# Performance work log

Measured on AMD Instinct MI355X. Metric: run time of the kernel, lower is better.

The kernel has to match this reference:

```python
import jax, jax.numpy as jnp
import numpy as np

N = 50000      # total nodes
E = 800000     # directed edges
G = 512        # graphs in batch
F_IN = 64      # node feature dim
H = 128        # hidden dim
L = 3          # gnn layers
OUT = 12       # tox21 tasks
EPS = 1e-5


def layer_norm(h, gamma, beta):
    mu = jnp.mean(h, axis=-1, keepdims=True)
    var = jnp.mean(jnp.square(h - mu), axis=-1, keepdims=True)
    return (h - mu) * jax.lax.rsqrt(var + EPS) * gamma + beta


def setup_inputs() -> dict:
    key = jax.random.key(0)
    ks = jax.random.split(key, 20)
    x = jax.random.normal(ks[0], (N, F_IN), jnp.float32)
    edge_index = jax.random.randint(ks[1], (2, E), 0, N, dtype=jnp.int64)
    batch_ids = jnp.sort(jax.random.randint(ks[2], (N,), 0, G, dtype=jnp.int64))
    s_in = 1.0 / np.sqrt(F_IN)
    s_h = 1.0 / np.sqrt(H)
    return {
        "x": x,
        "edge_index": edge_index,
        "batch_ids": batch_ids,
        "W_embed": jax.random.normal(ks[3], (F_IN, H), jnp.float32) * s_in,
        "b_embed": jnp.zeros((H,), jnp.float32),
        "g_embed": jnp.ones((H,), jnp.float32),
        "be_embed": jnp.zeros((H,), jnp.float32),
        "W_conv": jax.random.normal(ks[4], (L, H, H), jnp.float32) * s_h,
        "b_conv": jnp.zeros((L, H), jnp.float32),
        "g_ln": jnp.ones((L, H), jnp.float32),
        "b_ln": jnp.zeros((L, H), jnp.float32),
        "W_r1": jax.random.normal(ks[5], (H, H // 2), jnp.float32) * s_h,
        "b_r1": jnp.zeros((H // 2,), jnp.float32),
        "W_r2": jax.random.normal(ks[6], (H // 2, OUT), jnp.float32) * (1.0 / np.sqrt(H // 2)),
        "b_r2": jnp.zeros((OUT,), jnp.float32),
    }


def reference(x, edge_index, batch_ids, W_embed, b_embed, g_embed, be_embed,
              W_conv, b_conv, g_ln, b_ln, W_r1, b_r1, W_r2, b_r2):
    n = x.shape[0]
    # node embedding: Linear -> LayerNorm -> ReLU (dropout = eval identity)
    h = jax.nn.relu(layer_norm(x @ W_embed + b_embed, g_embed, be_embed))

    # GCN normalization with self-loops (PyG GCNConv semantics)
    loop = jnp.arange(n, dtype=edge_index.dtype)
    src = jnp.concatenate([edge_index[0], loop])  # message sources
    dst = jnp.concatenate([edge_index[1], loop])  # message targets
    deg = jax.ops.segment_sum(jnp.ones_like(dst, dtype=h.dtype), dst, num_segments=N)
    dinv = jnp.where(deg > 0, jax.lax.rsqrt(deg), 0.0)
    norm = dinv[src] * dinv[dst]  # [E+N]

    for i in range(L):
        h_prev = h
        m = h @ W_conv[i]                                        # [N,H] linear first
        msg = m[src] * norm[:, None]                             # gather + scale
        agg = jax.ops.segment_sum(msg, dst, num_segments=N)      # scatter-add
        agg = agg + b_conv[i]                                    # bias after aggregation
        h = jax.nn.relu(layer_norm(agg, g_ln[i], b_ln[i])) + h_prev  # norm+relu+residual

    # global mean pooling per graph
    counts = jax.ops.segment_sum(jnp.ones((n,), h.dtype), batch_ids, num_segments=G)
    pooled = jax.ops.segment_sum(h, batch_ids, num_segments=G) / jnp.maximum(counts, 1.0)[:, None]

    # readout MLP
    r = jax.nn.relu(pooled @ W_r1 + b_r1)
    return r @ W_r2 + b_r2
```

## Files before the change

### kernel.cpp

```cpp
#include <hip/hip_runtime.h>

#define HDIM 128
#define FIN 64
#define EPS 1e-5f
#define ECH 2048
#define PITCH 64

typedef unsigned int uint;
typedef unsigned short ushort;
typedef __attribute__((ext_vector_type(8))) short bf16x8;
typedef __attribute__((ext_vector_type(4))) float f32x4;

__device__ __forceinline__ ushort f2bf(float f) {
    uint u = __float_as_uint(f);
    return (ushort)((u + 0x7fffu + ((u >> 16) & 1u)) >> 16);
}
__device__ __forceinline__ float bflo(uint u) { return __uint_as_float(u << 16); }
__device__ __forceinline__ float bfhi(uint u) { return __uint_as_float(u & 0xffff0000u); }

#define PART_OF(d) (((d) >> 4) & 7)

__global__ __launch_bounds__(256) void embed_fused(
    const float* __restrict__ x, const float* __restrict__ W,
    const float* __restrict__ b, const float* __restrict__ g,
    const float* __restrict__ be, ushort* __restrict__ hbf, int nrows,
    const int* __restrict__ src, const int* __restrict__ dst,
    int* __restrict__ fcnt, ushort* __restrict__ ell, int e,
    const float* __restrict__ Wc, ushort* __restrict__ Wt)
{
    int t = threadIdx.x;
    int gtid = blockIdx.x * 256 + t;
    if (gtid < 3 * HDIM * HDIM) {
        int l = gtid >> 14, rem = gtid & 16383;
        int k = rem >> 7, nn = rem & 127;
        Wt[(l << 14) + nn * HDIM + k] = f2bf(Wc[gtid]);
    }
    {
        int gpart = blockIdx.x & 7;
        int base2 = ((blockIdx.x >> 3) * ECH) >> 1;
        const int2* dst2 = (const int2*)dst;
        const int2* src2 = (const int2*)src;
#pragma unroll
        for (int i = 0; i < ECH / 2 / 256; i++) {
            int idx2 = base2 + t + i * 256;
            if (idx2 * 2 < e) {
                int2 dd = dst2[idx2];
                int2 ss = src2[idx2];
                if (PART_OF(dd.x) == gpart) {
                    int slot = atomicAdd(&fcnt[dd.x], 1);
                    if (slot < PITCH) ell[((size_t)dd.x << 6) + slot] = (ushort)ss.x;
                }
                if (idx2 * 2 + 1 < e && PART_OF(dd.y) == gpart) {
                    int slot = atomicAdd(&fcnt[dd.y], 1);
                    if (slot < PITCH) ell[((size_t)dd.y << 6) + slot] = (ushort)ss.y;
                }
            }
        }
    }

    int row0 = blockIdx.x * 32;
    if (row0 >= nrows) return;

    __shared__ ushort Ws[FIN * HDIM];
    __shared__ ushort xs[32 * FIN];
    {
        const float4* W4 = (const float4*)W;
        ushort4* Ws4 = (ushort4*)Ws;
#pragma unroll
        for (int i = 0; i < (FIN * HDIM / 4) / 256; i++) {
            float4 v = W4[t + i * 256];
            ushort4 o = { f2bf(v.x), f2bf(v.y), f2bf(v.z), f2bf(v.w) };
            Ws4[t + i * 256] = o;
        }
    }
    int nr = nrows - row0; if (nr > 32) nr = 32;
    {
        const float4* x4 = (const float4*)(x + (size_t)row0 * FIN);
        ushort4* xs4 = (ushort4*)xs;
        for (int i = t; i < nr * (FIN / 4); i += 256) {
            float4 v = x4[i];
            ushort4 o = { f2bf(v.x), f2bf(v.y), f2bf(v.z), f2bf(v.w) };
            xs4[i] = o;
        }
    }
    __syncthreads();

    int c = (t & 31) * 4;
    int r0 = (t >> 5) * 4;
    float acc[4][4];
    float4 bv = *(const float4*)(b + c);
#pragma unroll
    for (int i = 0; i < 4; i++) { acc[i][0] = bv.x; acc[i][1] = bv.y; acc[i][2] = bv.z; acc[i][3] = bv.w; }
#pragma unroll 8
    for (int k = 0; k < FIN; k++) {
        uint2 wu = *(const uint2*)(Ws + k * HDIM + c);
        float w0 = bflo(wu.x), w1 = bfhi(wu.x), w2 = bflo(wu.y), w3 = bfhi(wu.y);
#pragma unroll
        for (int i = 0; i < 4; i++) {
            float xv = __uint_as_float((uint)xs[(r0 + i) * FIN + k] << 16);
            acc[i][0] += xv * w0; acc[i][1] += xv * w1;
            acc[i][2] += xv * w2; acc[i][3] += xv * w3;
        }
    }
    float4 gv = *(const float4*)(g + c);
    float4 bev = *(const float4*)(be + c);
#pragma unroll
    for (int i = 0; i < 4; i++) {
        float s1 = acc[i][0] + acc[i][1] + acc[i][2] + acc[i][3];
        float s2 = acc[i][0]*acc[i][0] + acc[i][1]*acc[i][1] + acc[i][2]*acc[i][2] + acc[i][3]*acc[i][3];
#pragma unroll
        for (int m = 16; m; m >>= 1) { s1 += __shfl_xor(s1, m); s2 += __shfl_xor(s2, m); }
        float mu = s1 * (1.0f / HDIM);
        float var = s2 * (1.0f / HDIM) - mu * mu;
        float rstd = rsqrtf(var + EPS);
        int row = row0 + r0 + i;
        if (row < nrows) {
            float ox = fmaxf((acc[i][0] - mu) * rstd * gv.x + bev.x, 0.f);
            float oy = fmaxf((acc[i][1] - mu) * rstd * gv.y + bev.y, 0.f);
            float oz = fmaxf((acc[i][2] - mu) * rstd * gv.z + bev.z, 0.f);
            float ow = fmaxf((acc[i][3] - mu) * rstd * gv.w + bev.w, 0.f);
            uint2 hb;
            hb.x = ((uint)f2bf(oy) << 16) | f2bf(ox);
            hb.y = ((uint)f2bf(ow) << 16) | f2bf(oz);
            *(uint2*)(hbf + (size_t)row * HDIM + c) = hb;
        }
    }
}

__global__ __launch_bounds__(256) void gemm_mfma_kernel(
    const ushort* __restrict__ hbf, const ushort* __restrict__ Wt,
    const int* __restrict__ fcnt, ushort* __restrict__ mbf, int nrows)
{
    __shared__ ushort ws[64 * HDIM];
    int t = threadIdx.x;
    int wid = t >> 6, lane = t & 63;
    int row0 = (blockIdx.x >> 1) * 64;
    int colh = (blockIdx.x & 1) * 64;

#pragma unroll
    for (int it = 0; it < 4; it++) {
        int chunk = t * 4 + it;
        int r = chunk >> 4;
        int offb = (chunk & 15) * 16;
        uint4 d = *(const uint4*)(Wt + (size_t)(colh + r) * HDIM + (offb >> 1));
        *(uint4*)((char*)ws + r * 256 + (offb ^ ((r & 7) << 4))) = d;
    }

    int arow = row0 + wid * 16 + (lane & 15);
    int arcl = (arow < nrows) ? arow : (nrows - 1);
    int kgrp = lane >> 4;
    const ushort* aptr = hbf + (size_t)arcl * HDIM + kgrp * 8;
    bf16x8 af[4];
#pragma unroll
    for (int ks = 0; ks < 4; ks++)
        af[ks] = *(const bf16x8*)(aptr + ks * 32);

    __syncthreads();

    f32x4 acc[4];
#pragma unroll
    for (int nt = 0; nt < 4; nt++) acc[nt] = (f32x4){0.f, 0.f, 0.f, 0.f};

    int kgb = kgrp * 16;
#pragma unroll
    for (int ks = 0; ks < 4; ks++) {
        int kb = ks * 64 + kgb;
#pragma unroll
        for (int nt = 0; nt < 4; nt++) {
            int nrow = nt * 16 + (lane & 15);
            bf16x8 bfrag = *(const bf16x8*)((const char*)ws + nrow * 256 + (kb ^ ((nrow & 7) << 4)));
            acc[nt] = __builtin_amdgcn_mfma_f32_16x16x32_bf16(af[ks], bfrag, acc[nt], 0, 0, 0);
        }
    }

    int rbase = row0 + wid * 16 + ((lane >> 4) << 2);
#pragma unroll
    for (int q = 0; q < 4; q++) {
        int grow = rbase + q;
        if (grow < nrows) {
            float dv = rsqrtf((float)(fcnt[grow] + 1));
            ushort* orow = mbf + (size_t)grow * HDIM + colh + (lane & 15);
#pragma unroll
            for (int nt = 0; nt < 4; nt++)
                orow[nt * 16] = f2bf(acc[nt][q] * dv);
        }
    }
}

__global__ __launch_bounds__(256) void agg_kernel(
    const ushort* __restrict__ mbf, const ushort* __restrict__ ell, const int* __restrict__ fcnt,
    const float* __restrict__ bc,
    const float* __restrict__ gl, const float* __restrict__ bl,
    const ushort* __restrict__ hbf_in, ushort* __restrict__ hbf_out, int n)
{
    int wave = threadIdx.x >> 6, lane = threadIdx.x & 63;
    int v = blockIdx.x * 4 + wave;
    if (v >= n) return;
    const uint* m1 = (const uint*)mbf;
    uint hp = ((const uint*)hbf_in)[(size_t)v * 64 + lane];
    uint aa = m1[(size_t)v * 64 + lane];
    float ax = bflo(aa), ay = bfhi(aa);
    int deg = fcnt[v];
    const ushort* row = ell + ((size_t)v << 6);
    for (int base = 0; base < deg; base += 64) {
        int idx = base + lane;
        int my = (idx < deg) ? (int)row[idx] : 0;
        int cc = deg - base; if (cc > 64) cc = 64;
        int i = 0;
        for (; i + 4 <= cc; i += 4) {
            int u0 = __shfl(my, i);
            int u1 = __shfl(my, i + 1);
            int u2 = __shfl(my, i + 2);
            int u3 = __shfl(my, i + 3);
            uint w0 = m1[(size_t)u0 * 64 + lane];
            uint w1 = m1[(size_t)u1 * 64 + lane];
            uint w2 = m1[(size_t)u2 * 64 + lane];
            uint w3 = m1[(size_t)u3 * 64 + lane];
            ax += bflo(w0); ay += bfhi(w0);
            ax += bflo(w1); ay += bfhi(w1);
            ax += bflo(w2); ay += bfhi(w2);
            ax += bflo(w3); ay += bfhi(w3);
        }
        for (; i < cc; ++i) {
            int u0 = __shfl(my, i);
            uint w0 = m1[(size_t)u0 * 64 + lane];
            ax += bflo(w0); ay += bfhi(w0);
        }
    }
    float dvv = rsqrtf((float)(deg + 1));
    float2 bcv = ((const float2*)bc)[lane];
    float vx = ax * dvv + bcv.x;
    float vy = ay * dvv + bcv.y;
    float s1v = vx + vy, s2v = vx * vx + vy * vy;
#pragma unroll
    for (int m = 32; m; m >>= 1) { s1v += __shfl_xor(s1v, m); s2v += __shfl_xor(s2v, m); }
    float mu = s1v * (1.f / 128.f);
    float var = s2v * (1.f / 128.f) - mu * mu;
    float rstd = rsqrtf(var + EPS);
    float2 gv = ((const float2*)gl)[lane];
    float2 blv = ((const float2*)bl)[lane];
    float ox = fmaxf((vx - mu) * rstd * gv.x + blv.x, 0.f) + bflo(hp);
    float oy = fmaxf((vy - mu) * rstd * gv.y + blv.y, 0.f) + bfhi(hp);
    ((uint*)hbf_out)[(size_t)v * 64 + lane] = ((uint)f2bf(oy) << 16) | f2bf(ox);
}

__global__ __launch_bounds__(256) void pool_readout(
    const ushort* __restrict__ hbf, const int* __restrict__ batch,
    const float* __restrict__ W1, const float* __restrict__ b1,
    const float* __restrict__ W2, const float* __restrict__ b2,
    float* __restrict__ out, int n, int G)
{
    int g = blockIdx.x, t = threadIdx.x;
    int lo = 0, hi = n;
    while (lo < hi) { int mid = (lo + hi) >> 1; if (batch[mid] < g) lo = mid + 1; else hi = mid; }
    int lo2 = lo, hi2 = n;
    while (lo2 < hi2) { int mid = (lo2 + hi2) >> 1; if (batch[mid] < g + 1) lo2 = mid + 1; else hi2 = mid; }
    int cp = t & 63, portion = t >> 6;
    float accx = 0.f, accy = 0.f;
    const uint* h1 = (const uint*)hbf;
    for (int nd = lo + portion; nd < lo2; nd += 4) {
        uint u = h1[(size_t)nd * 64 + cp];
        accx += bflo(u); accy += bfhi(u);
    }
    float cntf = (float)(lo2 - lo); if (cntf < 1.f) cntf = 1.f;
    __shared__ float psx[256], psy[256];
    __shared__ float ps[HDIM];
    __shared__ float rs[64];
    psx[t] = accx; psy[t] = accy;
    __syncthreads();
    if (t < 64) {
        float px = psx[t] + psx[t + 64] + psx[t + 128] + psx[t + 192];
        float py = psy[t] + psy[t + 64] + psy[t + 128] + psy[t + 192];
        ps[2 * t]     = px / cntf;
        ps[2 * t + 1] = py / cntf;
    }
    __syncthreads();
    if (t < 64) {
        float a = b1[t];
#pragma unroll 4
        for (int k = 0; k < HDIM; k++) a += ps[k] * W1[k * 64 + t];
        rs[t] = fmaxf(a, 0.f);
    }
    __syncthreads();
    if (t < 12) {
        float a = b2[t];
#pragma unroll
        for (int k = 0; k < 64; k++) a += rs[k] * W2[k * 12 + t];
        out[(size_t)g * 12 + t] = a;
    }
}

extern "C" void kernel_launch(void* const* d_in, const int* in_sizes, int n_in,
                              void* d_out, int out_size, void* d_ws, size_t ws_size,
                              hipStream_t stream) {
    const float* x       = (const float*)d_in[0];
    const int*   ei      = (const int*)d_in[1];
    const int*   batch   = (const int*)d_in[2];
    const float* W_embed = (const float*)d_in[3];
    const float* b_embed = (const float*)d_in[4];
    const float* g_embed = (const float*)d_in[5];
    const float* be_emb  = (const float*)d_in[6];
    const float* W_conv  = (const float*)d_in[7];
    const float* b_conv  = (const float*)d_in[8];
    const float* g_ln    = (const float*)d_in[9];
    const float* b_ln    = (const float*)d_in[10];
    const float* W_r1    = (const float*)d_in[11];
    const float* b_r1    = (const float*)d_in[12];
    const float* W_r2    = (const float*)d_in[13];
    const float* b_r2    = (const float*)d_in[14];
    float* out = (float*)d_out;

    int N = in_sizes[2];
    int E = in_sizes[1] / 2;
    int G = out_size / 12;
    int npad = ((N + 255) / 256) * 256;

    char* w = (char*)d_ws;
    ushort* hbf0 = (ushort*)w;  w += (size_t)N * HDIM * 2;
    ushort* hbf1 = (ushort*)w;  w += (size_t)N * HDIM * 2;
    ushort* mbf  = (ushort*)w;  w += (size_t)N * HDIM * 2;
    ushort* Wt   = (ushort*)w;  w += (size_t)3 * HDIM * HDIM * 2;
    int* fcnt    = (int*)w;     w += (size_t)npad * 4;
    ushort* ell  = (ushort*)w;  w += (size_t)npad * PITCH * 2;

    int nchunks = (E + ECH - 1) / ECH;
    int gridEC = nchunks * 8;
    int gemmBlocks = ((N + 63) / 64) * 2;

    hipMemsetAsync(fcnt, 0, (size_t)npad * 4, stream);

    embed_fused<<<gridEC, 256, 0, stream>>>(
        x, W_embed, b_embed, g_embed, be_emb, hbf0, N,
        ei, ei + E, fcnt, ell, E, W_conv, Wt);

    const ushort* hin = hbf0;
    ushort* hout = hbf1;
    for (int l = 0; l < 3; l++) {
        gemm_mfma_kernel<<<gemmBlocks, 256, 0, stream>>>(
            hin, Wt + (size_t)l * HDIM * HDIM, fcnt, mbf, N);
        agg_kernel<<<(N + 3) / 4, 256, 0, stream>>>(
            mbf, ell, fcnt, b_conv + l * HDIM, g_ln + l * HDIM, b_ln + l * HDIM,
            hin, hout, N);
        ushort* tmp = (ushort*)hin; hin = hout; hout = tmp;
    }
    pool_readout<<<G, 256, 0, stream>>>(hbf1 == hout ? hbf0 : hbf1, batch, W_r1, b_r1, W_r2, b_r2, out, N, G);
}
```

Before: 219.5 us.

## Build ELL adjacency via two-pass LDS counting sort instead of global atomics

Replaces the per-edge global atomicAdd on fcnt with a two-pass scheme. Pass one counts destinations per (chunk, partition) in shared memory. A scan kernel computes per-chunk base offsets and degrees, and pass two fills the ELL slots using LDS atomics, fused with the first-layer GEMM. This removes the memset and contended global atomics, and makes slot order deterministic. The cost is an extra kernel launch, extra count/base buffers, and two reads of the dst array.

Measured after the change: 256.0 us. 16.6% more time.

```diff
diff --git a/kernel.cpp b/kernel.cpp
--- a/kernel.cpp
+++ b/kernel.cpp
@@ -3,8 +3,9 @@
 #define HDIM 128
 #define FIN 64
 #define EPS 1e-5f
-#define ECH 2048
 #define PITCH 64
+#define NSUB 32
+#define NFB 256
 
 typedef unsigned int uint;
 typedef unsigned short ushort;
@@ -19,50 +20,45 @@
 __device__ __forceinline__ float bfhi(uint u) { return __uint_as_float(u & 0xffff0000u); }
 
 #define PART_OF(d) (((d) >> 4) & 7)
-
-__global__ __launch_bounds__(256) void embed_fused(
+#define DLOCAL(d)  (((((d) >> 7)) << 4) | ((d) & 15))
+
+__global__ __launch_bounds__(256) void embed_pass1(
     const float* __restrict__ x, const float* __restrict__ W,
     const float* __restrict__ b, const float* __restrict__ g,
     const float* __restrict__ be, ushort* __restrict__ hbf, int nrows,
-    const int* __restrict__ src, const int* __restrict__ dst,
-    int* __restrict__ fcnt, ushort* __restrict__ ell, int e,
+    const int* __restrict__ dst, int* __restrict__ cnt32, int e, int chunkLen, int DL,
     const float* __restrict__ Wc, ushort* __restrict__ Wt)
 {
+    extern __shared__ char smem[];
     int t = threadIdx.x;
-    int gtid = blockIdx.x * 256 + t;
-    if (gtid < 3 * HDIM * HDIM) {
-        int l = gtid >> 14, rem = gtid & 16383;
-        int k = rem >> 7, nn = rem & 127;
-        Wt[(l << 14) + nn * HDIM + k] = f2bf(Wc[gtid]);
-    }
-    {
-        int gpart = blockIdx.x & 7;
-        int base2 = ((blockIdx.x >> 3) * ECH) >> 1;
-        const int2* dst2 = (const int2*)dst;
-        const int2* src2 = (const int2*)src;
-#pragma unroll
-        for (int i = 0; i < ECH / 2 / 256; i++) {
-            int idx2 = base2 + t + i * 256;
-            if (idx2 * 2 < e) {
-                int2 dd = dst2[idx2];
-                int2 ss = src2[idx2];
-                if (PART_OF(dd.x) == gpart) {
-                    int slot = atomicAdd(&fcnt[dd.x], 1);
-                    if (slot < PITCH) ell[((size_t)dd.x << 6) + slot] = (ushort)ss.x;
-                }
-                if (idx2 * 2 + 1 < e && PART_OF(dd.y) == gpart) {
-                    int slot = atomicAdd(&fcnt[dd.y], 1);
-                    if (slot < PITCH) ell[((size_t)dd.y << 6) + slot] = (ushort)ss.y;
-                }
-            }
-        }
-    }
-
-    int row0 = blockIdx.x * 32;
+
+    if ((int)blockIdx.x < NFB) {
+        int gtid = blockIdx.x * 256 + t;
+        if (gtid < 3 * HDIM * HDIM) {
+            int l = gtid >> 14, rem = gtid & 16383;
+            int k = rem >> 7, nn = rem & 127;
+            Wt[(l << 14) + nn * HDIM + k] = f2bf(Wc[gtid]);
+        }
+        int* cnt = (int*)smem;
+        for (int i = t; i < DL; i += 256) cnt[i] = 0;
+        __syncthreads();
+        int gp = blockIdx.x & 7, s = blockIdx.x >> 3;
+        int beg = s * chunkLen, end = beg + chunkLen; if (end > e) end = e;
+        for (int idx = beg + t; idx < end; idx += 256) {
+            int d = dst[idx];
+            if (PART_OF(d) == gp) atomicAdd(&cnt[DLOCAL(d)], 1);
+        }
+        __syncthreads();
+        int* outp = cnt32 + (size_t)blockIdx.x * DL;
+        for (int i = t; i < DL; i += 256) outp[i] = cnt[i];
+        return;
+    }
+
+    int row0 = ((int)blockIdx.x - NFB) * 32;
     if (row0 >= nrows) return;
 
-    __shared__ ushort Ws[FIN * HDIM];
-    __shared__ ushort xs[32 * FIN];
+    ushort* Ws = (ushort*)smem;
+    ushort* xs = (ushort*)(smem + 16384);
     {
         const float4* W4 = (const float4*)W;
         ushort4* Ws4 = (ushort4*)Ws;
@@ -127,15 +123,33 @@
     }
 }
 
-__global__ __launch_bounds__(256) void gemm_mfma_kernel(
+__global__ __launch_bounds__(256) void scan_b(
+    const int* __restrict__ cnt32, int* __restrict__ base32,
+    int* __restrict__ fcnt, int n, int DL)
+{
+    int d = blockIdx.x * 256 + threadIdx.x;
+    if (d >= n) return;
+    int gp = PART_OF(d), dl = DLOCAL(d);
+    int run = 0;
+#pragma unroll
+    for (int s = 0; s < NSUB; s++) {
+        size_t off = (size_t)((s << 3) | gp) * DL + dl;
+        int cv = cnt32[off];
+        base32[off] = run;
+        run += cv;
+    }
+    fcnt[d] = run;
+}
+
+__device__ __forceinline__ void gemm_body(
     const ushort* __restrict__ hbf, const ushort* __restrict__ Wt,
-    const int* __restrict__ fcnt, ushort* __restrict__ mbf, int nrows)
-{
-    __shared__ ushort ws[64 * HDIM];
+    const int* __restrict__ fcnt, ushort* __restrict__ mbf, int nrows,
+    int bid, ushort* ws)
+{
     int t = threadIdx.x;
     int wid = t >> 6, lane = t & 63;
-    int row0 = (blockIdx.x >> 1) * 64;
-    int colh = (blockIdx.x & 1) * 64;
+    int row0 = (bid >> 1) * 64;
+    int colh = (bid & 1) * 64;
 
 #pragma unroll
     for (int it = 0; it < 4; it++) {
@@ -185,6 +199,42 @@
                 orow[nt * 16] = f2bf(acc[nt][q] * dv);
         }
     }
+}
+
+__global__ __launch_bounds__(256) void pass2_gemm0(
+    const int* __restrict__ src, const int* __restrict__ dst,
+    const int* __restrict__ base32, ushort* __restrict__ ell,
+    int e, int chunkLen, int DL,
+    const ushort* __restrict__ hbf, const ushort* __restrict__ Wt,
+    const int* __restrict__ fcnt, ushort* __restrict__ mbf, int nrows)
+{
+    extern __shared__ char smem[];
+    int t = threadIdx.x;
+    if ((int)blockIdx.x < NFB) {
+        int* slot = (int*)smem;
+        const int* brow = base32 + (size_t)blockIdx.x * DL;
+        for (int i = t; i < DL; i += 256) slot[i] = brow[i];
+        __syncthreads();
+        int gp = blockIdx.x & 7, s = blockIdx.x >> 3;
+        int beg = s * chunkLen, end = beg + chunkLen; if (end > e) end = e;
+        for (int idx = beg + t; idx < end; idx += 256) {
+            int d = dst[idx];
+            if (PART_OF(d) == gp) {
+                int sl = atomicAdd(&slot[DLOCAL(d)], 1);
+                if (sl < PITCH) ell[((size_t)d << 6) + sl] = (ushort)src[idx];
+            }
+        }
+        return;
+    }
+    gemm_body(hbf, Wt, fcnt, mbf, nrows, (int)blockIdx.x - NFB, (ushort*)smem);
+}
+
+__global__ __launch_bounds__(256) void gemm_mfma_kernel(
+    const ushort* __restrict__ hbf, const ushort* __restrict__ Wt,
+    const int* __restrict__ fcnt, ushort* __restrict__ mbf, int nrows)
+{
+    __shared__ ushort ws[64 * HDIM];
+    gemm_body(hbf, Wt, fcnt, mbf, nrows, (int)blockIdx.x, ws);
 }
 
 __global__ __launch_bounds__(256) void agg_kernel(
@@ -201,11 +251,12 @@
     uint aa = m1[(size_t)v * 64 + lane];
     float ax = bflo(aa), ay = bfhi(aa);
     int deg = fcnt[v];
+    int degl = deg < PITCH ? deg : PITCH;
     const ushort* row = ell + ((size_t)v << 6);
-    for (int base = 0; base < deg; base += 64) {
+    for (int base = 0; base < degl; base += 64) {
         int idx = base + lane;
-        int my = (idx < deg) ? (int)row[idx] : 0;
-        int cc = deg - base; if (cc > 64) cc = 64;
+        int my = (idx < degl) ? (int)row[idx] : 0;
+        int cc = degl - base; if (cc > 64) cc = 64;
         int i = 0;
         for (; i + 4 <= cc; i += 4) {
             int u0 = __shfl(my, i);
@@ -314,6 +365,8 @@
     int E = in_sizes[1] / 2;
     int G = out_size / 12;
     int npad = ((N + 255) / 256) * 256;
+    int DL = ((N >> 7) + 1) * 16;
+    int chunkLen = (E + NSUB - 1) / NSUB;
 
     char* w = (char*)d_ws;
     ushort* hbf0 = (ushort*)w;  w += (size_t)N * HDIM * 2;
@@ -321,27 +374,31 @@
     ushort* mbf  = (ushort*)w;  w += (size_t)N * HDIM * 2;
     ushort* Wt   = (ushort*)w;  w += (size_t)3 * HDIM * HDIM * 2;
     int* fcnt    = (int*)w;     w += (size_t)npad * 4;
+    int* cnt32   = (int*)w;     w += (size_t)NFB * DL * 4;
+    int* base32  = (int*)w;     w += (size_t)NFB * DL * 4;
     ushort* ell  = (ushort*)w;  w += (size_t)npad * PITCH * 2;
 
-    int nchunks = (E + ECH - 1) / ECH;
-    int gridEC = nchunks * 8;
+    int embedBlocks = (N + 31) / 32;
     int gemmBlocks = ((N + 63) / 64) * 2;
-
-    hipMemsetAsync(fcnt, 0, (size_t)npad * 4, stream);
-
-    embed_fused<<<gridEC, 256, 0, stream>>>(
+    size_t dyn1 = (size_t)(DL * 4 > 20480 ? DL * 4 : 20480);
+    size_t dyn3 = (size_t)(DL * 4 > 16384 ? DL * 4 : 16384);
+
+    embed_pass1<<<NFB + embedBlocks, 256, dyn1, stream>>>(
         x, W_embed, b_embed, g_embed, be_emb, hbf0, N,
-        ei, ei + E, fcnt, ell, E, W_conv, Wt);
-
-    const ushort* hin = hbf0;
-    ushort* hout = hbf1;
-    for (int l = 0; l < 3; l++) {
-        gemm_mfma_kernel<<<gemmBlocks, 256, 0, stream>>>(
-            hin, Wt + (size_t)l * HDIM * HDIM, fcnt, mbf, N);
-        agg_kernel<<<(N + 3) / 4, 256, 0, stream>>>(
-            mbf, ell, fcnt, b_conv + l * HDIM, g_ln + l * HDIM, b_ln + l * HDIM,
-            hin, hout, N);
-        ushort* tmp = (ushort*)hin; hin = hout; hout = tmp;
-    }
-    pool_readout<<<G, 256, 0, stream>>>(hbf1 == hout ? hbf0 : hbf1, batch, W_r1, b_r1, W_r2, b_r2, out, N, G);
-}
+        ei + E, cnt32, E, chunkLen, DL, W_conv, Wt);
+    scan_b<<<(N + 255) / 256, 256, 0, stream>>>(cnt32, base32, fcnt, N, DL);
+    pass2_gemm0<<<NFB + gemmBlocks, 256, dyn3, stream>>>(
+        ei, ei + E, base32, ell, E, chunkLen, DL,
+        hbf0, Wt, fcnt, mbf, N);
+
+    agg_kernel<<<(N + 3) / 4, 256, 0, stream>>>(
+        mbf, ell, fcnt, b_conv, g_ln, b_ln, hbf0, hbf1, N);
+    gemm_mfma_kernel<<<gemmBlocks, 256, 0, stream>>>(hbf1, Wt + (size_t)1 * HDIM * HDIM, fcnt, mbf, N);
+    agg_kernel<<<(N + 3) / 4, 256, 0, stream>>>(
+        mbf, ell, fcnt, b_conv + HDIM, g_ln + HDIM, b_ln + HDIM, hbf1, hbf0, N);
+    gemm_mfma_kernel<<<gemmBlocks, 256, 0, stream>>>(hbf0, Wt + (size_t)2 * HDIM * HDIM, fcnt, mbf, N);
+    agg_kernel<<<(N + 3) / 4, 256, 0, stream>>>(
+        mbf, ell, fcnt, b_conv + 2 * HDIM, g_ln + 2 * HDIM, b_ln + 2 * HDIM, hbf0, hbf1, N);
+
+    pool_readout<<<G, 256, 0, stream>>>(hbf1, batch, W_r1, b_r1, W_r2, b_r2, out, N, G);
+}
```
